# Optimization experiments

Hardware: AMD Instinct MI355X
Metric: run time of the kernel (lower is better)

The kernel has to match this reference:

```python
import jax, jax.numpy as jnp
import numpy as np
from jax import lax

BN_EPS = 1e-5


def _gate(x, w, g, b, m, v):
    """ZPool -> 7x7 conv (2->1 ch) -> BN (eval) -> sigmoid -> multiply. x: [B,C,H,W]."""
    z = jnp.concatenate(
        [x.max(axis=1, keepdims=True), x.mean(axis=1, keepdims=True)], axis=1
    )  # [B,2,H,W]
    y = lax.conv_general_dilated(
        z, w, window_strides=(1, 1), padding=((3, 3), (3, 3)),
        dimension_numbers=("NCHW", "OIHW", "NCHW"),
    )  # [B,1,H,W]
    y = (y - m) * lax.rsqrt(v + BN_EPS) * g + b
    return x * jax.nn.sigmoid(y)


def setup_inputs() -> dict:
    key = jax.random.key(0)
    ks = jax.random.split(key, 4)
    B, C, H, W = 32, 256, 56, 56
    return {
        "x": jax.random.normal(ks[0], (B, C, H, W), dtype=jnp.float32),
        "w_ch": jax.random.normal(ks[1], (1, 2, 7, 7), dtype=jnp.float32),
        "w_cw": jax.random.normal(ks[2], (1, 2, 7, 7), dtype=jnp.float32),
        "w_hw": jax.random.normal(ks[3], (1, 2, 7, 7), dtype=jnp.float32),
        "gamma": jnp.ones((3,), jnp.float32),
        "beta": jnp.zeros((3,), jnp.float32),
        "mean": jnp.zeros((3,), jnp.float32),
        "var": jnp.ones((3,), jnp.float32),
    }


def reference(x, w_ch, w_cw, w_hw, gamma, beta, mean, var):
    # Branch 1: swap C<->H -> gate -> swap back
    x_ch = jnp.transpose(x, (0, 2, 1, 3))
    x_ch = jnp.transpose(_gate(x_ch, w_ch, gamma[0], beta[0], mean[0], var[0]), (0, 2, 1, 3))
    # Branch 2: swap C<->W -> gate -> swap back
    x_cw = jnp.transpose(x, (0, 3, 2, 1))
    x_cw = jnp.transpose(_gate(x_cw, w_cw, gamma[1], beta[1], mean[1], var[1]), (0, 3, 2, 1))
    # Branch 3: identity spatial gate
    x_hw = _gate(x, w_hw, gamma[2], beta[2], mean[2], var[2])
    return (x_ch + x_cw + x_hw) / 3.0
```

## Files before the change

### kernel.cpp

```cpp
#include <hip/hip_runtime.h>
#include <math.h>


#define B_ 32
#define C_ 256
#define H_ 56
#define W_ 56
#define HW_ 3136
#define LDSW 60
#define NPOOLC (B_ * 49 * 2)
#define NPOOLHW (B_ * C_)

__global__ __launch_bounds__(256) void pool_all(const float* __restrict__ x,
                                                float* __restrict__ P1,
                                                float* __restrict__ P2,
                                                float* __restrict__ P3p) {
    __shared__ float sm[H_ * LDSW];
    const int t = threadIdx.x;
    const int bid = blockIdx.x;

    if (bid < NPOOLC) {
        const int chunk = bid & 1;
        const int rest = bid >> 1;
        const int b = rest / 49;
        const int tile = rest - b * 49;
        const int lane = t & 63, wv = t >> 6;
        const int hw = tile * 64 + lane;
        const float* src = x + (size_t)b * C_ * HW_ + (size_t)(chunk * 128 + wv * 32) * HW_ + hw;

        float m0 = -INFINITY, m1 = -INFINITY, s0 = 0.f, s1a = 0.f;
#pragma unroll
        for (int i = 0; i < 16; ++i) {
            float v0 = src[(size_t)(2 * i) * HW_];
            float v1 = src[(size_t)(2 * i + 1) * HW_];
            m0 = fmaxf(m0, v0); s0 += v0;
            m1 = fmaxf(m1, v1); s1a += v1;
        }
        float m = fmaxf(m0, m1), s = s0 + s1a;

        float* lm = sm;
        float* ls = sm + 256;
        lm[wv * 64 + lane] = m; ls[wv * 64 + lane] = s;
        __syncthreads();
        if (wv == 0) {
#pragma unroll
            for (int k = 1; k < 4; ++k) {
                m = fmaxf(m, lm[k * 64 + lane]); s += ls[k * 64 + lane];
            }
            P3p[(((size_t)b * 2 + chunk) * 2 + 0) * HW_ + hw] = m;
            P3p[(((size_t)b * 2 + chunk) * 2 + 1) * HW_ + hw] = s;
        }
    } else {
        const int bid2 = bid - NPOOLC;
        const int b = bid2 >> 8;
        const int c = bid2 & 255;
        const float* src = x + (size_t)bid2 * HW_;

        float4 v0 = ((const float4*)src)[t];
        float4 v1 = ((const float4*)src)[t + 256];
        float4 v2 = ((const float4*)src)[t + 512];
        float4 v3 = (t < 16) ? ((const float4*)src)[t + 768] : make_float4(0, 0, 0, 0);
        {
            int h0 = t / 14, w0 = (t - h0 * 14) * 4;
            *(float4*)&sm[h0 * LDSW + w0] = v0;
            int v = t + 256; int h1 = v / 14, w1 = (v - h1 * 14) * 4;
            *(float4*)&sm[h1 * LDSW + w1] = v1;
            v = t + 512; int h2 = v / 14, w2 = (v - h2 * 14) * 4;
            *(float4*)&sm[h2 * LDSW + w2] = v2;
            if (t < 16) {
                v = t + 768; int h3 = v / 14, w3 = (v - h3 * 14) * 4;
                *(float4*)&sm[h3 * LDSW + w3] = v3;
            }
        }
        __syncthreads();

        if (t < 224) {
            const int q = t & 3;
            {
                const int h = t >> 2;
                float m = -INFINITY, s = 0.f;
#pragma unroll
                for (int j = 0; j < 14; ++j) {
                    float v = sm[h * LDSW + q + 4 * j];
                    m = fmaxf(m, v); s += v;
                }
                m = fmaxf(m, __shfl_down(m, 1)); s += __shfl_down(s, 1);
                m = fmaxf(m, __shfl_down(m, 2)); s += __shfl_down(s, 2);
                if (q == 0) {
                    P2[(((size_t)b * 2 + 0) * H_ + h) * C_ + c] = m;
                    P2[(((size_t)b * 2 + 1) * H_ + h) * C_ + c] = s * (1.f / 56.f);
                }
            }
            {
                const int w = t >> 2;
                float m = -INFINITY, s = 0.f;
#pragma unroll
                for (int j = 0; j < 14; ++j) {
                    float v = sm[(q * 14 + j) * LDSW + w];
                    m = fmaxf(m, v); s += v;
                }
                m = fmaxf(m, __shfl_down(m, 1)); s += __shfl_down(s, 1);
                m = fmaxf(m, __shfl_down(m, 2)); s += __shfl_down(s, 2);
                if (q == 0) {
                    P1[(((size_t)b * 2 + 0) * C_ + c) * W_ + w] = m;
                    P1[(((size_t)b * 2 + 1) * C_ + c) * W_ + w] = s * (1.f / 56.f);
                }
            }
        }
    }
}

__global__ __launch_bounds__(256) void conv_all(const float* __restrict__ P1,
                                                const float* __restrict__ P2,
                                                const float* __restrict__ P3p,
                                                const float* __restrict__ w_ch,
                                                const float* __restrict__ w_cw,
                                                const float* __restrict__ w_hw,
                                                const float* __restrict__ gamma,
                                                const float* __restrict__ beta,
                                                const float* __restrict__ mean,
                                                const float* __restrict__ var,
                                                float* __restrict__ s1,
                                                float* __restrict__ s2,
                                                float* __restrict__ s3) {
    const int k = blockIdx.z;
    const float* Z; const float* wsrc; float* S; int A, D;
    if (k == 0)      { Z = P1;  wsrc = w_ch; S = s1; A = C_; D = W_; }
    else if (k == 1) { Z = P2;  wsrc = w_cw; S = s2; A = H_; D = C_; }
    else             { Z = P3p; wsrc = w_hw; S = s3; A = H_; D = W_; }

    __shared__ float wl[98];
    const int t = threadIdx.x;
    if (t < 98) wl[t] = wsrc[t];
    __syncthreads();

    const int b = blockIdx.y;
    const int AD = A * D;
    const int idx = blockIdx.x * 256 + t;
    if (idx >= AD) return;
    const int a = idx / D;
    const int d = idx - a * D;

    float acc = 0.f;
    if (k < 2) {
        const float* Z0 = Z + (size_t)b * 2 * AD;
#pragma unroll
        for (int dy = 0; dy < 7; ++dy) {
            int aa = a + dy - 3;
            if (aa < 0 || aa >= A) continue;
#pragma unroll
            for (int dx = 0; dx < 7; ++dx) {
                int dd = d + dx - 3;
                if (dd < 0 || dd >= D) continue;
                acc += Z0[aa * D + dd] * wl[dy * 7 + dx]
                     + Z0[AD + aa * D + dd] * wl[49 + dy * 7 + dx];
            }
        }
    } else {
        const float* Zm0 = Z + (((size_t)b * 2 + 0) * 2 + 0) * HW_;
        const float* Zs0 = Z + (((size_t)b * 2 + 0) * 2 + 1) * HW_;
        const float* Zm1 = Z + (((size_t)b * 2 + 1) * 2 + 0) * HW_;
        const float* Zs1 = Z + (((size_t)b * 2 + 1) * 2 + 1) * HW_;
#pragma unroll
        for (int dy = 0; dy < 7; ++dy) {
            int aa = a + dy - 3;
            if (aa < 0 || aa >= A) continue;
#pragma unroll
            for (int dx = 0; dx < 7; ++dx) {
                int dd = d + dx - 3;
                if (dd < 0 || dd >= D) continue;
                int o = aa * D + dd;
                float zmax = fmaxf(Zm0[o], Zm1[o]);
                float zmean = (Zs0[o] + Zs1[o]) * (1.f / 256.f);
                acc += zmax * wl[dy * 7 + dx] + zmean * wl[49 + dy * 7 + dx];
            }
        }
    }
    float y = (acc - mean[k]) * rsqrtf(var[k] + 1e-5f) * gamma[k] + beta[k];
    S[(size_t)b * AD + idx] = 1.f / (1.f + expf(-y));
}

__global__ __launch_bounds__(256) void final_mul(const float* __restrict__ x,
                                                 const float* __restrict__ s1,
                                                 const float* __restrict__ s2,
                                                 const float* __restrict__ s3,
                                                 float* __restrict__ out) {
    const int vid = blockIdx.x * 256 + threadIdx.x;
    const int p = vid / 784;
    const int r = vid - p * 784;
    const int h = r / 14;
    const int w4 = (r - h * 14) << 2;
    const int b = p >> 8;
    const int c = p & 255;

    const size_t xoff = (size_t)p * HW_ + h * 56 + w4;
    const float4 xv = *(const float4*)(x + xoff);
    const float4 s1v = *(const float4*)(s1 + ((size_t)(b * C_ + c)) * W_ + w4);
    const float s2s = s2[((size_t)b * H_ + h) * C_ + c];
    const float4 s3v = *(const float4*)(s3 + ((size_t)b * H_ + h) * W_ + w4);

    float4 o;
    o.x = xv.x * (s1v.x + s2s + s3v.x) * (1.f / 3.f);
    o.y = xv.y * (s1v.y + s2s + s3v.y) * (1.f / 3.f);
    o.z = xv.z * (s1v.z + s2s + s3v.z) * (1.f / 3.f);
    o.w = xv.w * (s1v.w + s2s + s3v.w) * (1.f / 3.f);
    *(float4*)(out + xoff) = o;
}

extern "C" void kernel_launch(void* const* d_in, const int* in_sizes, int n_in,
                              void* d_out, int out_size, void* d_ws, size_t ws_size,
                              hipStream_t stream) {
    const float* x = (const float*)d_in[0];
    const float* w_ch = (const float*)d_in[1];
    const float* w_cw = (const float*)d_in[2];
    const float* w_hw = (const float*)d_in[3];
    const float* gamma = (const float*)d_in[4];
    const float* beta = (const float*)d_in[5];
    const float* mean = (const float*)d_in[6];
    const float* var = (const float*)d_in[7];
    float* out = (float*)d_out;

    float* ws = (float*)d_ws;
    float* P1 = ws;
    float* P2 = P1 + 917504;
    float* P3p = P2 + 917504;
    float* s1 = P3p + 401408;
    float* s2 = s1 + 458752;
    float* s3 = s2 + 458752;

    pool_all<<<NPOOLC + NPOOLHW, 256, 0, stream>>>(x, P1, P2, P3p);
    conv_all<<<dim3(56, B_, 3), 256, 0, stream>>>(P1, P2, P3p, w_ch, w_cw, w_hw,
                                                  gamma, beta, mean, var, s1, s2, s3);
    final_mul<<<(B_ * C_ * HW_) / 4 / 256, 256, 0, stream>>>(x, s1, s2, s3, out);
}
```

Measured before the change: 264.1 us.

## Fuse channel and spatial pooling into one pass over x with partial combine

```diff
diff --git a/kernel.cpp b/kernel.cpp
--- a/kernel.cpp
+++ b/kernel.cpp
@@ -8,72 +8,59 @@
 #define W_ 56
 #define HW_ 3136
 #define LDSW 60
-#define NPOOLC (B_ * 49 * 2)
-#define NPOOLHW (B_ * C_)
-
-__global__ __launch_bounds__(256) void pool_all(const float* __restrict__ x,
-                                                float* __restrict__ P1,
-                                                float* __restrict__ P2,
-                                                float* __restrict__ P3p) {
-    __shared__ float sm[H_ * LDSW];
+#define CG 8
+#define NGRP (C_ / CG)
+
+__device__ __forceinline__ float4 f4max(float4 a, float4 b) {
+    return make_float4(fmaxf(a.x, b.x), fmaxf(a.y, b.y), fmaxf(a.z, b.z), fmaxf(a.w, b.w));
+}
+__device__ __forceinline__ float4 f4add(float4 a, float4 b) {
+    return make_float4(a.x + b.x, a.y + b.y, a.z + b.z, a.w + b.w);
+}
+
+__global__ __launch_bounds__(256) void pool_fused(const float* __restrict__ x,
+                                                  float* __restrict__ P1,
+                                                  float* __restrict__ P2,
+                                                  float* __restrict__ P3p) {
+    __shared__ float smem[H_ * LDSW];
     const int t = threadIdx.x;
-    const int bid = blockIdx.x;
-
-    if (bid < NPOOLC) {
-        const int chunk = bid & 1;
-        const int rest = bid >> 1;
-        const int b = rest / 49;
-        const int tile = rest - b * 49;
-        const int lane = t & 63, wv = t >> 6;
-        const int hw = tile * 64 + lane;
-        const float* src = x + (size_t)b * C_ * HW_ + (size_t)(chunk * 128 + wv * 32) * HW_ + hw;
-
-        float m0 = -INFINITY, m1 = -INFINITY, s0 = 0.f, s1a = 0.f;
-#pragma unroll
-        for (int i = 0; i < 16; ++i) {
-            float v0 = src[(size_t)(2 * i) * HW_];
-            float v1 = src[(size_t)(2 * i + 1) * HW_];
-            m0 = fmaxf(m0, v0); s0 += v0;
-            m1 = fmaxf(m1, v1); s1a += v1;
-        }
-        float m = fmaxf(m0, m1), s = s0 + s1a;
-
-        float* lm = sm;
-        float* ls = sm + 256;
-        lm[wv * 64 + lane] = m; ls[wv * 64 + lane] = s;
+    const int b = blockIdx.x >> 5;
+    const int g = blockIdx.x & (NGRP - 1);
+    const int c0 = g * CG;
+    const float* __restrict__ base = x + (size_t)(b * C_ + c0) * HW_;
+
+    const int s0 = t, s1i = t + 256, s2i = t + 512, s3i = t + 768;
+    const int h0 = s0 / 14,  ad0 = h0 * LDSW + (s0 - h0 * 14) * 4;
+    const int h1 = s1i / 14, ad1 = h1 * LDSW + (s1i - h1 * 14) * 4;
+    const int h2 = s2i / 14, ad2 = h2 * LDSW + (s2i - h2 * 14) * 4;
+    const int h3 = s3i / 14, ad3 = h3 * LDSW + (s3i - h3 * 14) * 4;
+
+    float4 mx0, mx1, mx2, mx3, su0, su1, su2, su3;
+    mx0 = mx1 = mx2 = mx3 = make_float4(-INFINITY, -INFINITY, -INFINITY, -INFINITY);
+    su0 = su1 = su2 = su3 = make_float4(0.f, 0.f, 0.f, 0.f);
+
+    const float4* bp = (const float4*)base;
+    float4 cur0 = bp[s0], cur1 = bp[s1i], cur2 = bp[s2i];
+    float4 cur3 = (t < 16) ? bp[s3i] : make_float4(0, 0, 0, 0);
+
+    for (int cc = 0; cc < CG; ++cc) {
+        float4 nx0, nx1, nx2, nx3;
+        if (cc < CG - 1) {
+            const float4* nb = (const float4*)(base + (size_t)(cc + 1) * HW_);
+            nx0 = nb[s0]; nx1 = nb[s1i]; nx2 = nb[s2i];
+            if (t < 16) nx3 = nb[s3i];
+        }
+        *(float4*)&smem[ad0] = cur0;
+        *(float4*)&smem[ad1] = cur1;
+        *(float4*)&smem[ad2] = cur2;
+        if (t < 16) *(float4*)&smem[ad3] = cur3;
+        mx0 = f4max(mx0, cur0); su0 = f4add(su0, cur0);
+        mx1 = f4max(mx1, cur1); su1 = f4add(su1, cur1);
+        mx2 = f4max(mx2, cur2); su2 = f4add(su2, cur2);
+        if (t < 16) { mx3 = f4max(mx3, cur3); su3 = f4add(su3, cur3); }
         __syncthreads();
-        if (wv == 0) {
-#pragma unroll
-            for (int k = 1; k < 4; ++k) {
-                m = fmaxf(m, lm[k * 64 + lane]); s += ls[k * 64 + lane];
-            }
-            P3p[(((size_t)b * 2 + chunk) * 2 + 0) * HW_ + hw] = m;
-            P3p[(((size_t)b * 2 + chunk) * 2 + 1) * HW_ + hw] = s;
-        }
-    } else {
-        const int bid2 = bid - NPOOLC;
-        const int b = bid2 >> 8;
-        const int c = bid2 & 255;
-        const float* src = x + (size_t)bid2 * HW_;
-
-        float4 v0 = ((const float4*)src)[t];
-        float4 v1 = ((const float4*)src)[t + 256];
-        float4 v2 = ((const float4*)src)[t + 512];
-        float4 v3 = (t < 16) ? ((const float4*)src)[t + 768] : make_float4(0, 0, 0, 0);
-        {
-            int h0 = t / 14, w0 = (t - h0 * 14) * 4;
-            *(float4*)&sm[h0 * LDSW + w0] = v0;
-            int v = t + 256; int h1 = v / 14, w1 = (v - h1 * 14) * 4;
-            *(float4*)&sm[h1 * LDSW + w1] = v1;
-            v = t + 512; int h2 = v / 14, w2 = (v - h2 * 14) * 4;
-            *(float4*)&sm[h2 * LDSW + w2] = v2;
-            if (t < 16) {
-                v = t + 768; int h3 = v / 14, w3 = (v - h3 * 14) * 4;
-                *(float4*)&sm[h3 * LDSW + w3] = v3;
-            }
-        }
-        __syncthreads();
-
+
+        const int c = c0 + cc;
         if (t < 224) {
             const int q = t & 3;
             {
@@ -81,7 +68,7 @@
                 float m = -INFINITY, s = 0.f;
 #pragma unroll
                 for (int j = 0; j < 14; ++j) {
-                    float v = sm[h * LDSW + q + 4 * j];
+                    float v = smem[h * LDSW + q + 4 * j];
                     m = fmaxf(m, v); s += v;
                 }
                 m = fmaxf(m, __shfl_down(m, 1)); s += __shfl_down(s, 1);
@@ -96,7 +83,7 @@
                 float m = -INFINITY, s = 0.f;
 #pragma unroll
                 for (int j = 0; j < 14; ++j) {
-                    float v = sm[(q * 14 + j) * LDSW + w];
+                    float v = smem[(q * 14 + j) * LDSW + w];
                     m = fmaxf(m, v); s += v;
                 }
                 m = fmaxf(m, __shfl_down(m, 1)); s += __shfl_down(s, 1);
@@ -107,12 +94,38 @@
                 }
             }
         }
+        __syncthreads();
+        if (cc < CG - 1) {
+            cur0 = nx0; cur1 = nx1; cur2 = nx2;
+            if (t < 16) cur3 = nx3;
+        }
     }
+    float4* Pm = (float4*)(P3p + ((size_t)(b * NGRP + g) * 2 + 0) * HW_);
+    float4* Ps = (float4*)(P3p + ((size_t)(b * NGRP + g) * 2 + 1) * HW_);
+    Pm[s0] = mx0; Pm[s1i] = mx1; Pm[s2i] = mx2;
+    Ps[s0] = su0; Ps[s1i] = su1; Ps[s2i] = su2;
+    if (t < 16) { Pm[s3i] = mx3; Ps[s3i] = su3; }
+}
+
+__global__ __launch_bounds__(256) void combine_p3(const float* __restrict__ P3p,
+                                                  float* __restrict__ P3) {
+    const int idx = blockIdx.x * 256 + threadIdx.x;
+    const int b = idx / HW_;
+    const int hw = idx - b * HW_;
+    const float* src = P3p + (size_t)b * NGRP * 2 * HW_ + hw;
+    float m = -INFINITY, s = 0.f;
+#pragma unroll
+    for (int gg = 0; gg < NGRP; ++gg) {
+        m = fmaxf(m, src[(size_t)(2 * gg + 0) * HW_]);
+        s += src[(size_t)(2 * gg + 1) * HW_];
+    }
+    P3[((size_t)b * 2 + 0) * HW_ + hw] = m;
+    P3[((size_t)b * 2 + 1) * HW_ + hw] = s * (1.f / 256.f);
 }
 
 __global__ __launch_bounds__(256) void conv_all(const float* __restrict__ P1,
                                                 const float* __restrict__ P2,
-                                                const float* __restrict__ P3p,
+                                                const float* __restrict__ P3,
                                                 const float* __restrict__ w_ch,
                                                 const float* __restrict__ w_cw,
                                                 const float* __restrict__ w_hw,
@@ -125,9 +138,9 @@
                                                 float* __restrict__ s3) {
     const int k = blockIdx.z;
     const float* Z; const float* wsrc; float* S; int A, D;
-    if (k == 0)      { Z = P1;  wsrc = w_ch; S = s1; A = C_; D = W_; }
-    else if (k == 1) { Z = P2;  wsrc = w_cw; S = s2; A = H_; D = C_; }
-    else             { Z = P3p; wsrc = w_hw; S = s3; A = H_; D = W_; }
+    if (k == 0)      { Z = P1; wsrc = w_ch; S = s1; A = C_; D = W_; }
+    else if (k == 1) { Z = P2; wsrc = w_cw; S = s2; A = H_; D = C_; }
+    else             { Z = P3; wsrc = w_hw; S = s3; A = H_; D = W_; }
 
     __shared__ float wl[98];
     const int t = threadIdx.x;
@@ -141,39 +154,18 @@
     const int a = idx / D;
     const int d = idx - a * D;
 
+    const float* Z0 = Z + (size_t)b * 2 * AD;
     float acc = 0.f;
-    if (k < 2) {
-        const float* Z0 = Z + (size_t)b * 2 * AD;
-#pragma unroll
-        for (int dy = 0; dy < 7; ++dy) {
-            int aa = a + dy - 3;
-            if (aa < 0 || aa >= A) continue;
-#pragma unroll
-            for (int dx = 0; dx < 7; ++dx) {
-                int dd = d + dx - 3;
-                if (dd < 0 || dd >= D) continue;
-                acc += Z0[aa * D + dd] * wl[dy * 7 + dx]
-                     + Z0[AD + aa * D + dd] * wl[49 + dy * 7 + dx];
-            }
-        }
-    } else {
-        const float* Zm0 = Z + (((size_t)b * 2 + 0) * 2 + 0) * HW_;
-        const float* Zs0 = Z + (((size_t)b * 2 + 0) * 2 + 1) * HW_;
-        const float* Zm1 = Z + (((size_t)b * 2 + 1) * 2 + 0) * HW_;
-        const float* Zs1 = Z + (((size_t)b * 2 + 1) * 2 + 1) * HW_;
-#pragma unroll
-        for (int dy = 0; dy < 7; ++dy) {
-            int aa = a + dy - 3;
-            if (aa < 0 || aa >= A) continue;
-#pragma unroll
-            for (int dx = 0; dx < 7; ++dx) {
-                int dd = d + dx - 3;
-                if (dd < 0 || dd >= D) continue;
-                int o = aa * D + dd;
-                float zmax = fmaxf(Zm0[o], Zm1[o]);
-                float zmean = (Zs0[o] + Zs1[o]) * (1.f / 256.f);
-                acc += zmax * wl[dy * 7 + dx] + zmean * wl[49 + dy * 7 + dx];
-            }
+#pragma unroll
+    for (int dy = 0; dy < 7; ++dy) {
+        int aa = a + dy - 3;
+        if (aa < 0 || aa >= A) continue;
+#pragma unroll
+        for (int dx = 0; dx < 7; ++dx) {
+            int dd = d + dx - 3;
+            if (dd < 0 || dd >= D) continue;
+            acc += Z0[aa * D + dd] * wl[dy * 7 + dx]
+                 + Z0[AD + aa * D + dd] * wl[49 + dy * 7 + dx];
         }
     }
     float y = (acc - mean[k]) * rsqrtf(var[k] + 1e-5f) * gamma[k] + beta[k];
@@ -224,12 +216,14 @@
     float* P1 = ws;
     float* P2 = P1 + 917504;
     float* P3p = P2 + 917504;
-    float* s1 = P3p + 401408;
+    float* P3 = P3p + 6422528;
+    float* s1 = P3 + 200704;
     float* s2 = s1 + 458752;
     float* s3 = s2 + 458752;
 
-    pool_all<<<NPOOLC + NPOOLHW, 256, 0, stream>>>(x, P1, P2, P3p);
-    conv_all<<<dim3(56, B_, 3), 256, 0, stream>>>(P1, P2, P3p, w_ch, w_cw, w_hw,
+    pool_fused<<<B_ * NGRP, 256, 0, stream>>>(x, P1, P2, P3p);
+    combine_p3<<<(B_ * HW_) / 256, 256, 0, stream>>>(P3p, P3);
+    conv_all<<<dim3(56, B_, 3), 256, 0, stream>>>(P1, P2, P3, w_ch, w_cw, w_hw,
                                                   gamma, beta, mean, var, s1, s2, s3);
     final_mul<<<(B_ * C_ * HW_) / 4 / 256, 256, 0, stream>>>(x, s1, s2, s3, out);
 }
```

Result: no change. 265.6 us (+0.6%).
